# Kernel optimization log

Hardware: AMD Instinct MI355X
Metric: run time of the kernel (lower is better)

The kernel has to match this reference:

```python
import jax, jax.numpy as jnp
import numpy as np

N_NODES = 10000
N_EDGES = 640000
HIDDEN = 128
OUT = 10

def setup_inputs() -> dict:
    key = jax.random.key(0)
    k1, k2, k3, k4 = jax.random.split(key, 4)
    x = jax.random.normal(k1, (N_NODES, HIDDEN), dtype=jnp.float32)
    edge_index = jax.random.randint(k2, (2, N_EDGES), 0, N_NODES, dtype=jnp.int64)
    # ClassifierMLP2 params: Linear(2*hidden -> hidden) -> ReLU -> Linear(hidden -> out)
    W1 = jax.random.normal(k3, (2 * HIDDEN, HIDDEN), dtype=jnp.float32) / np.sqrt(2 * HIDDEN)
    b1 = jnp.zeros((HIDDEN,), dtype=jnp.float32)
    W2 = jax.random.normal(k4, (HIDDEN, OUT), dtype=jnp.float32) / np.sqrt(HIDDEN)
    b2 = jnp.zeros((OUT,), dtype=jnp.float32)
    return {"x": x, "edge_index": edge_index, "W1": W1, "b1": b1, "W2": W2, "b2": b2}

def reference(x, edge_index, W1, b1, W2, b2):
    # mix_node_features(..., node_feat_mixing='cat'): gather src/dst node
    # embeddings per edge and concatenate along feature dim -> [E, 2*H]
    src, dst = edge_index[0], edge_index[1]
    edges_x = jnp.concatenate([x[src], x[dst]], axis=-1)  # [E, 2H]
    # ClassifierMLP2 (dropout inactive at inference)
    h = jax.nn.relu(edges_x @ W1 + b1)                    # [E, H]
    return h @ W2 + b2                                    # [E, OUT]
```

## Files before the change

kernel.cpp:

```cpp
#include <hip/hip_runtime.h>


typedef _Float16 f16;
typedef _Float16 f16x8 __attribute__((ext_vector_type(8)));
typedef float    f32x4 __attribute__((ext_vector_type(4)));

#define HID  128
#define TWOH 256
#define OUTD 10

__global__ __launch_bounds__(256) void node_AB(
    const float* __restrict__ x,
    const float* __restrict__ W1,
    const float* __restrict__ b1,
    f16* __restrict__ AB,
    int n_nodes)
{
    const int t = threadIdx.x;
    const int lane = t & 63;
    const int r = lane & 15, g = lane >> 4;
    const int wv = t >> 6;
    const int n0 = blockIdx.x * 16;
    const int c0 = wv * 64;

    f16x8 w1f[4][4];
#pragma unroll
    for (int ct = 0; ct < 4; ++ct) {
        const int c = c0 + ct * 16 + r;
        const float* wp = (c < HID) ? (W1 + c) : (W1 + HID * HID + (c - HID));
#pragma unroll
        for (int st = 0; st < 4; ++st) {
            f16x8 v;
#pragma unroll
            for (int j = 0; j < 8; ++j)
                v[j] = (f16)wp[(long)(st * 32 + g * 8 + j) * HID];
            w1f[ct][st] = v;
        }
    }

    const int xrow = (n0 + r < n_nodes) ? (n0 + r) : (n_nodes - 1);
    f32x4 acc[4] = {{0,0,0,0},{0,0,0,0},{0,0,0,0},{0,0,0,0}};
#pragma unroll
    for (int st = 0; st < 4; ++st) {
        const float* xp = x + (long)xrow * HID + st * 32 + g * 8;
        const float4 x0 = *(const float4*)xp;
        const float4 x1 = *(const float4*)(xp + 4);
        f16x8 a;
        a[0] = (f16)x0.x; a[1] = (f16)x0.y; a[2] = (f16)x0.z; a[3] = (f16)x0.w;
        a[4] = (f16)x1.x; a[5] = (f16)x1.y; a[6] = (f16)x1.z; a[7] = (f16)x1.w;
#pragma unroll
        for (int ct = 0; ct < 4; ++ct)
            acc[ct] = __builtin_amdgcn_mfma_f32_16x16x32_f16(a, w1f[ct][st], acc[ct], 0, 0, 0);
    }

#pragma unroll
    for (int ct = 0; ct < 4; ++ct) {
        const int c = c0 + ct * 16 + r;
        const float bias = (c < HID) ? b1[c] : 0.f;
#pragma unroll
        for (int q = 0; q < 4; ++q) {
            const int node = n0 + g * 4 + q;
            if (node < n_nodes)
                AB[(long)node * TWOH + c] = (f16)(acc[ct][q] + bias);
        }
    }
}

__global__ __launch_bounds__(256) void edge_mlp(
    const f16* __restrict__ AB,
    const int* __restrict__ ei,
    const float* __restrict__ W2,
    const float* __restrict__ b2,
    float* __restrict__ out,
    int n_edges)
{
    const int t = threadIdx.x;
    const int lane = t & 63;
    const int r = lane & 15, g = lane >> 4;
    const int wv = t >> 6;

    const bool cok = (r < OUTD);
    const int cw = cok ? r : 0;
    f16x8 w2f[4];
#pragma unroll
    for (int st = 0; st < 4; ++st) {
        f16x8 v;
#pragma unroll
        for (int j = 0; j < 8; ++j) {
            const float w = W2[(long)(st * 32 + g * 8 + j) * OUTD + cw];
            v[j] = cok ? (f16)w : (f16)0.f;
        }
        w2f[st] = v;
    }
    const float bj = cok ? b2[r] : 0.f;

    const f16x8* __restrict__ ABv = (const f16x8*)AB;
    const long eb = (long)blockIdx.x * 256 + wv * 64;

#pragma unroll
    for (int it = 0; it < 4; ++it) {
        const long e = eb + it * 16 + r;
        const long ec = (e < n_edges) ? e : (n_edges - 1);
        const int sn = ei[ec];
        const int dn = ei[(long)n_edges + ec];

        f32x4 acc = {0, 0, 0, 0};
#pragma unroll
        for (int st = 0; st < 4; ++st) {
            const f16x8 a = ABv[(long)sn * 32 + st * 4 + g];
            const f16x8 c = ABv[(long)dn * 32 + 16 + st * 4 + g];
            f16x8 s = a + c;
            const f16x8 z = {0, 0, 0, 0, 0, 0, 0, 0};
            s = __builtin_elementwise_max(s, z);
            acc = __builtin_amdgcn_mfma_f32_16x16x32_f16(s, w2f[st], acc, 0, 0, 0);
        }

        if (cok) {
            const long er = eb + it * 16 + g * 4;
#pragma unroll
            for (int q = 0; q < 4; ++q) {
                const long ee = er + q;
                if (ee < n_edges)
                    out[ee * OUTD + r] = acc[q] + bj;
            }
        }
    }
}

extern "C" void kernel_launch(void* const* d_in, const int* in_sizes, int n_in,
                              void* d_out, int out_size, void* d_ws, size_t ws_size,
                              hipStream_t stream) {
    const float* x  = (const float*)d_in[0];
    const int*   ei = (const int*)d_in[1];
    const float* W1 = (const float*)d_in[2];
    const float* b1 = (const float*)d_in[3];
    const float* W2 = (const float*)d_in[4];
    const float* b2 = (const float*)d_in[5];
    float* out = (float*)d_out;

    const int n_nodes = in_sizes[0] / HID;
    const int n_edges = in_sizes[1] / 2;

    f16* AB = (f16*)d_ws;

    node_AB<<<(n_nodes + 15) / 16, 256, 0, stream>>>(x, W1, b1, AB, n_nodes);

    edge_mlp<<<(n_edges + 255) / 256, 256, 0, stream>>>(AB, ei, W2, b2, out, n_edges);
}
```

Before: 70.60 us.

## Prepack fp16 weight fragments and software-pipeline edge gathers

A small kernel converts W1 and W2 once per call into fp16 MFMA fragment order. The node and edge kernels then load those fragments with vector loads instead of doing strided scalar fp32 loads and converts in every block. The edge kernel now handles 8 tiles of 16 edges per wave. It preloads all indices and keeps gathers several tiles ahead of the MFMA compute, with sched_barriers to hide gather latency. This adds a third kernel launch, raises register pressure, and uses occupancy hints of 3 blocks.

Result: faster. 61.78 us (-12.5%).

```diff
diff --git a/kernel.cpp b/kernel.cpp
--- a/kernel.cpp
+++ b/kernel.cpp
@@ -9,9 +9,42 @@
 #define TWOH 256
 #define OUTD 10
 
-__global__ __launch_bounds__(256) void node_AB(
+__global__ __launch_bounds__(256) void prep_weights(
+    const float* __restrict__ W1,
+    const float* __restrict__ W2,
+    f16* __restrict__ W1P,
+    f16* __restrict__ W2P)
+{
+    const int slot = blockIdx.x * 256 + threadIdx.x;
+    if (slot < 4096) {
+        const int lane = slot & 63, i = slot >> 6;
+        const int r = lane & 15, g = lane >> 4;
+        const int wv = i >> 4, ct = (i >> 2) & 3, st = i & 3;
+        const int c = wv * 64 + ct * 16 + r;
+        f16x8 v;
+#pragma unroll
+        for (int j = 0; j < 8; ++j) {
+            const int k = st * 32 + g * 8 + j;
+            const float w = (c < HID) ? W1[k * HID + c]
+                                      : W1[(HID + k) * HID + (c - HID)];
+            v[j] = (f16)w;
+        }
+        *(f16x8*)(W1P + (long)slot * 8) = v;
+    } else if (slot < 4096 + 256) {
+        const int s2 = slot - 4096;
+        const int lane = s2 & 63, st = s2 >> 6;
+        const int r = lane & 15, g = lane >> 4;
+        f16x8 v;
+#pragma unroll
+        for (int j = 0; j < 8; ++j)
+            v[j] = (r < OUTD) ? (f16)W2[(st * 32 + g * 8 + j) * OUTD + r] : (f16)0.f;
+        *(f16x8*)(W2P + (long)s2 * 8) = v;
+    }
+}
+
+__global__ __launch_bounds__(256, 3) void node_AB(
     const float* __restrict__ x,
-    const float* __restrict__ W1,
+    const f16* __restrict__ W1P,
     const float* __restrict__ b1,
     f16* __restrict__ AB,
     int n_nodes)
@@ -21,33 +54,35 @@
     const int r = lane & 15, g = lane >> 4;
     const int wv = t >> 6;
     const int n0 = blockIdx.x * 16;
-    const int c0 = wv * 64;
-
-    f16x8 w1f[4][4];
-#pragma unroll
-    for (int ct = 0; ct < 4; ++ct) {
-        const int c = c0 + ct * 16 + r;
-        const float* wp = (c < HID) ? (W1 + c) : (W1 + HID * HID + (c - HID));
-#pragma unroll
-        for (int st = 0; st < 4; ++st) {
-            f16x8 v;
-#pragma unroll
-            for (int j = 0; j < 8; ++j)
-                v[j] = (f16)wp[(long)(st * 32 + g * 8 + j) * HID];
-            w1f[ct][st] = v;
-        }
-    }
 
     const int xrow = (n0 + r < n_nodes) ? (n0 + r) : (n_nodes - 1);
-    f32x4 acc[4] = {{0,0,0,0},{0,0,0,0},{0,0,0,0},{0,0,0,0}};
+    float4 xl[4][2];
 #pragma unroll
     for (int st = 0; st < 4; ++st) {
         const float* xp = x + (long)xrow * HID + st * 32 + g * 8;
-        const float4 x0 = *(const float4*)xp;
-        const float4 x1 = *(const float4*)(xp + 4);
+        xl[st][0] = *(const float4*)xp;
+        xl[st][1] = *(const float4*)(xp + 4);
+    }
+
+    f16x8 w1f[4][4];
+    float bias[4];
+#pragma unroll
+    for (int ct = 0; ct < 4; ++ct) {
+        const int c = wv * 64 + ct * 16 + r;
+        bias[ct] = (c < HID) ? b1[c] : 0.f;
+#pragma unroll
+        for (int st = 0; st < 4; ++st)
+            w1f[ct][st] = *(const f16x8*)(W1P + ((long)((wv * 16 + ct * 4 + st)) * 64 + lane) * 8);
+    }
+
+    f32x4 acc[4] = {{0,0,0,0},{0,0,0,0},{0,0,0,0},{0,0,0,0}};
+#pragma unroll
+    for (int st = 0; st < 4; ++st) {
         f16x8 a;
-        a[0] = (f16)x0.x; a[1] = (f16)x0.y; a[2] = (f16)x0.z; a[3] = (f16)x0.w;
-        a[4] = (f16)x1.x; a[5] = (f16)x1.y; a[6] = (f16)x1.z; a[7] = (f16)x1.w;
+        a[0] = (f16)xl[st][0].x; a[1] = (f16)xl[st][0].y;
+        a[2] = (f16)xl[st][0].z; a[3] = (f16)xl[st][0].w;
+        a[4] = (f16)xl[st][1].x; a[5] = (f16)xl[st][1].y;
+        a[6] = (f16)xl[st][1].z; a[7] = (f16)xl[st][1].w;
 #pragma unroll
         for (int ct = 0; ct < 4; ++ct)
             acc[ct] = __builtin_amdgcn_mfma_f32_16x16x32_f16(a, w1f[ct][st], acc[ct], 0, 0, 0);
@@ -55,21 +90,20 @@
 
 #pragma unroll
     for (int ct = 0; ct < 4; ++ct) {
-        const int c = c0 + ct * 16 + r;
-        const float bias = (c < HID) ? b1[c] : 0.f;
+        const int c = wv * 64 + ct * 16 + r;
 #pragma unroll
         for (int q = 0; q < 4; ++q) {
             const int node = n0 + g * 4 + q;
             if (node < n_nodes)
-                AB[(long)node * TWOH + c] = (f16)(acc[ct][q] + bias);
+                AB[(long)node * TWOH + c] = (f16)(acc[ct][q] + bias[ct]);
         }
     }
 }
 
-__global__ __launch_bounds__(256) void edge_mlp(
+__global__ __launch_bounds__(256, 3) void edge_mlp(
     const f16* __restrict__ AB,
     const int* __restrict__ ei,
-    const float* __restrict__ W2,
+    const f16* __restrict__ W2P,
     const float* __restrict__ b2,
     float* __restrict__ out,
     int n_edges)
@@ -79,52 +113,80 @@
     const int r = lane & 15, g = lane >> 4;
     const int wv = t >> 6;
 
-    const bool cok = (r < OUTD);
-    const int cw = cok ? r : 0;
     f16x8 w2f[4];
 #pragma unroll
-    for (int st = 0; st < 4; ++st) {
-        f16x8 v;
-#pragma unroll
-        for (int j = 0; j < 8; ++j) {
-            const float w = W2[(long)(st * 32 + g * 8 + j) * OUTD + cw];
-            v[j] = cok ? (f16)w : (f16)0.f;
-        }
-        w2f[st] = v;
-    }
-    const float bj = cok ? b2[r] : 0.f;
+    for (int st = 0; st < 4; ++st)
+        w2f[st] = *(const f16x8*)(W2P + ((long)st * 64 + lane) * 8);
+    const int rc = (r < OUTD) ? r : 0;
+    const float bj = b2[rc];
 
     const f16x8* __restrict__ ABv = (const f16x8*)AB;
-    const long eb = (long)blockIdx.x * 256 + wv * 64;
-
-#pragma unroll
-    for (int it = 0; it < 4; ++it) {
+    const long eb = (long)blockIdx.x * 512 + wv * 128;
+
+    int sn[8], dn[8];
+#pragma unroll
+    for (int it = 0; it < 8; ++it) {
         const long e = eb + it * 16 + r;
         const long ec = (e < n_edges) ? e : (n_edges - 1);
-        const int sn = ei[ec];
-        const int dn = ei[(long)n_edges + ec];
-
-        f32x4 acc = {0, 0, 0, 0};
-#pragma unroll
-        for (int st = 0; st < 4; ++st) {
-            const f16x8 a = ABv[(long)sn * 32 + st * 4 + g];
-            const f16x8 c = ABv[(long)dn * 32 + 16 + st * 4 + g];
-            f16x8 s = a + c;
-            const f16x8 z = {0, 0, 0, 0, 0, 0, 0, 0};
-            s = __builtin_elementwise_max(s, z);
-            acc = __builtin_amdgcn_mfma_f32_16x16x32_f16(s, w2f[st], acc, 0, 0, 0);
-        }
-
-        if (cok) {
-            const long er = eb + it * 16 + g * 4;
-#pragma unroll
-            for (int q = 0; q < 4; ++q) {
-                const long ee = er + q;
-                if (ee < n_edges)
-                    out[ee * OUTD + r] = acc[q] + bj;
-            }
-        }
-    }
+        sn[it] = ei[ec];
+        dn[it] = ei[(long)n_edges + ec];
+    }
+
+    const f16x8 zt = {0, 0, 0, 0, 0, 0, 0, 0};
+
+#define GATHER(Pa, Pc, IT)                                                  \
+    f16x8 Pa[4], Pc[4];                                                     \
+    {                                                                       \
+        const long ab_ = (long)sn[IT] * 32, bb_ = (long)dn[IT] * 32;        \
+        _Pragma("unroll")                                                   \
+        for (int st = 0; st < 4; ++st) {                                    \
+            Pa[st] = ABv[ab_ + st * 4 + g];                                 \
+            Pc[st] = ABv[bb_ + 16 + st * 4 + g];                            \
+        }                                                                   \
+    }
+
+#define COMPSTORE(Pa, Pc, IT)                                               \
+    {                                                                       \
+        f32x4 acc = {0, 0, 0, 0};                                           \
+        _Pragma("unroll")                                                   \
+        for (int st = 0; st < 4; ++st) {                                    \
+            const f16x8 s = __builtin_elementwise_max(Pa[st] + Pc[st], zt); \
+            acc = __builtin_amdgcn_mfma_f32_16x16x32_f16(s, w2f[st], acc, 0, 0, 0); \
+        }                                                                   \
+        if (r < OUTD) {                                                     \
+            _Pragma("unroll")                                               \
+            for (int q = 0; q < 4; ++q) {                                   \
+                const long ee = eb + IT * 16 + g * 4 + q;                   \
+                if (ee < n_edges) out[ee * OUTD + r] = acc[q] + bj;         \
+            }                                                               \
+        }                                                                   \
+    }
+
+    GATHER(a0, c0, 0)
+    GATHER(a1, c1, 1)
+    GATHER(a2, c2, 2)
+    __builtin_amdgcn_sched_barrier(0);
+    COMPSTORE(a0, c0, 0)
+    GATHER(a3, c3, 3)
+    __builtin_amdgcn_sched_barrier(0);
+    COMPSTORE(a1, c1, 1)
+    GATHER(a4, c4, 4)
+    __builtin_amdgcn_sched_barrier(0);
+    COMPSTORE(a2, c2, 2)
+    GATHER(a5, c5, 5)
+    __builtin_amdgcn_sched_barrier(0);
+    COMPSTORE(a3, c3, 3)
+    GATHER(a6, c6, 6)
+    __builtin_amdgcn_sched_barrier(0);
+    COMPSTORE(a4, c4, 4)
+    GATHER(a7, c7, 7)
+    __builtin_amdgcn_sched_barrier(0);
+    COMPSTORE(a5, c5, 5)
+    COMPSTORE(a6, c6, 6)
+    COMPSTORE(a7, c7, 7)
+
+#undef GATHER
+#undef COMPSTORE
 }
 
 extern "C" void kernel_launch(void* const* d_in, const int* in_sizes, int n_in,
@@ -141,9 +203,13 @@
     const int n_nodes = in_sizes[0] / HID;
     const int n_edges = in_sizes[1] / 2;
 
-    f16* AB = (f16*)d_ws;
-
-    node_AB<<<(n_nodes + 15) / 16, 256, 0, stream>>>(x, W1, b1, AB, n_nodes);
-
-    edge_mlp<<<(n_edges + 255) / 256, 256, 0, stream>>>(AB, ei, W2, b2, out, n_edges);
-}
+    f16* AB  = (f16*)d_ws;
+    f16* W1P = AB + (long)n_nodes * TWOH;
+    f16* W2P = W1P + 4096 * 8;
+
+    prep_weights<<<17, 256, 0, stream>>>(W1, W2, W1P, W2P);
+
+    node_AB<<<(n_nodes + 15) / 16, 256, 0, stream>>>(x, W1P, b1, AB, n_nodes);
+
+    edge_mlp<<<(n_edges + 511) / 512, 256, 0, stream>>>(AB, ei, W2P, b2, out, n_edges);
+}
```

## Prepack weights into fp16 MFMA fragments and shrink per-block work in both kernels

Applied to the files above, without the earlier changes.

Adds a small kernel that converts W1 and W2 once per call into fp16 fragments already laid out for MFMA, so node and edge kernels load them with one vector load per lane instead of strided scalar fp32 loads. node_AB now splits output columns across four times as many blocks, each wave computing a single 16-column tile. edge_mlp handles one 16-edge tile per wave and issues all eight gather loads up front for more memory-level parallelism, with launch bounds raised for occupancy. This costs an extra kernel launch, more blocks that each re-read x, and the weight prep on every call.

Measured after the change: 69.87 us. Within noise of the previous version (-1.0%).

```diff
diff --git a/kernel.cpp b/kernel.cpp
--- a/kernel.cpp
+++ b/kernel.cpp
@@ -9,9 +9,42 @@
 #define TWOH 256
 #define OUTD 10
 
-__global__ __launch_bounds__(256) void node_AB(
+__global__ __launch_bounds__(256) void prep_weights(
+    const float* __restrict__ W1,
+    const float* __restrict__ W2,
+    f16* __restrict__ W1P,
+    f16* __restrict__ W2P)
+{
+    const int slot = blockIdx.x * 256 + threadIdx.x;
+    if (slot < 4096) {
+        const int lane = slot & 63, i = slot >> 6;
+        const int r = lane & 15, g = lane >> 4;
+        const int T = i >> 2, st = i & 3;
+        const int c = T * 16 + r;
+        f16x8 v;
+#pragma unroll
+        for (int j = 0; j < 8; ++j) {
+            const int k = st * 32 + g * 8 + j;
+            const float w = (c < HID) ? W1[k * HID + c]
+                                      : W1[(HID + k) * HID + (c - HID)];
+            v[j] = (f16)w;
+        }
+        *(f16x8*)(W1P + (long)slot * 8) = v;
+    } else if (slot < 4096 + 256) {
+        const int s2 = slot - 4096;
+        const int lane = s2 & 63, st = s2 >> 6;
+        const int r = lane & 15, g = lane >> 4;
+        f16x8 v;
+#pragma unroll
+        for (int j = 0; j < 8; ++j)
+            v[j] = (r < OUTD) ? (f16)W2[(st * 32 + g * 8 + j) * OUTD + r] : (f16)0.f;
+        *(f16x8*)(W2P + (long)s2 * 8) = v;
+    }
+}
+
+__global__ __launch_bounds__(256, 6) void node_AB(
     const float* __restrict__ x,
-    const float* __restrict__ W1,
+    const f16* __restrict__ W1P,
     const float* __restrict__ b1,
     f16* __restrict__ AB,
     int n_nodes)
@@ -20,56 +53,48 @@
     const int lane = t & 63;
     const int r = lane & 15, g = lane >> 4;
     const int wv = t >> 6;
-    const int n0 = blockIdx.x * 16;
-    const int c0 = wv * 64;
-
-    f16x8 w1f[4][4];
-#pragma unroll
-    for (int ct = 0; ct < 4; ++ct) {
-        const int c = c0 + ct * 16 + r;
-        const float* wp = (c < HID) ? (W1 + c) : (W1 + HID * HID + (c - HID));
-#pragma unroll
-        for (int st = 0; st < 4; ++st) {
-            f16x8 v;
-#pragma unroll
-            for (int j = 0; j < 8; ++j)
-                v[j] = (f16)wp[(long)(st * 32 + g * 8 + j) * HID];
-            w1f[ct][st] = v;
-        }
-    }
+    const int n0 = (blockIdx.x >> 2) * 16;
+    const int T = (blockIdx.x & 3) * 4 + wv;
+    const int c = T * 16 + r;
 
     const int xrow = (n0 + r < n_nodes) ? (n0 + r) : (n_nodes - 1);
-    f32x4 acc[4] = {{0,0,0,0},{0,0,0,0},{0,0,0,0},{0,0,0,0}};
+    float4 xl[4][2];
 #pragma unroll
     for (int st = 0; st < 4; ++st) {
         const float* xp = x + (long)xrow * HID + st * 32 + g * 8;
-        const float4 x0 = *(const float4*)xp;
-        const float4 x1 = *(const float4*)(xp + 4);
+        xl[st][0] = *(const float4*)xp;
+        xl[st][1] = *(const float4*)(xp + 4);
+    }
+
+    f16x8 w1f[4];
+#pragma unroll
+    for (int st = 0; st < 4; ++st)
+        w1f[st] = *(const f16x8*)(W1P + ((long)(T * 4 + st) * 64 + lane) * 8);
+    const float bias = (c < HID) ? b1[c] : 0.f;
+
+    f32x4 acc = {0, 0, 0, 0};
+#pragma unroll
+    for (int st = 0; st < 4; ++st) {
         f16x8 a;
-        a[0] = (f16)x0.x; a[1] = (f16)x0.y; a[2] = (f16)x0.z; a[3] = (f16)x0.w;
-        a[4] = (f16)x1.x; a[5] = (f16)x1.y; a[6] = (f16)x1.z; a[7] = (f16)x1.w;
-#pragma unroll
-        for (int ct = 0; ct < 4; ++ct)
-            acc[ct] = __builtin_amdgcn_mfma_f32_16x16x32_f16(a, w1f[ct][st], acc[ct], 0, 0, 0);
+        a[0] = (f16)xl[st][0].x; a[1] = (f16)xl[st][0].y;
+        a[2] = (f16)xl[st][0].z; a[3] = (f16)xl[st][0].w;
+        a[4] = (f16)xl[st][1].x; a[5] = (f16)xl[st][1].y;
+        a[6] = (f16)xl[st][1].z; a[7] = (f16)xl[st][1].w;
+        acc = __builtin_amdgcn_mfma_f32_16x16x32_f16(a, w1f[st], acc, 0, 0, 0);
     }
 
 #pragma unroll
-    for (int ct = 0; ct < 4; ++ct) {
-        const int c = c0 + ct * 16 + r;
-        const float bias = (c < HID) ? b1[c] : 0.f;
-#pragma unroll
-        for (int q = 0; q < 4; ++q) {
-            const int node = n0 + g * 4 + q;
-            if (node < n_nodes)
-                AB[(long)node * TWOH + c] = (f16)(acc[ct][q] + bias);
-        }
+    for (int q = 0; q < 4; ++q) {
+        const int node = n0 + g * 4 + q;
+        if (node < n_nodes)
+            AB[(long)node * TWOH + c] = (f16)(acc[q] + bias);
     }
 }
 
-__global__ __launch_bounds__(256) void edge_mlp(
+__global__ __launch_bounds__(256, 6) void edge_mlp(
     const f16* __restrict__ AB,
     const int* __restrict__ ei,
-    const float* __restrict__ W2,
+    const f16* __restrict__ W2P,
     const float* __restrict__ b2,
     float* __restrict__ out,
     int n_edges)
@@ -79,50 +104,47 @@
     const int r = lane & 15, g = lane >> 4;
     const int wv = t >> 6;
 
-    const bool cok = (r < OUTD);
-    const int cw = cok ? r : 0;
+    const long eb = (long)blockIdx.x * 64 + wv * 16;
+    const long e = eb + r;
+    const long ec = (e < n_edges) ? e : (n_edges - 1);
+    const int sn = ei[ec];
+    const int dn = ei[(long)n_edges + ec];
+
+    const f16* pa = AB + ((long)sn * TWOH + g * 8);
+    const f16* pb = AB + ((long)dn * TWOH + HID + g * 8);
+    f16x8 a0 = *(const f16x8*)pa;
+    f16x8 a1 = *(const f16x8*)(pa + 32);
+    f16x8 a2 = *(const f16x8*)(pa + 64);
+    f16x8 a3 = *(const f16x8*)(pa + 96);
+    f16x8 c0 = *(const f16x8*)pb;
+    f16x8 c1 = *(const f16x8*)(pb + 32);
+    f16x8 c2 = *(const f16x8*)(pb + 64);
+    f16x8 c3 = *(const f16x8*)(pb + 96);
+
     f16x8 w2f[4];
 #pragma unroll
-    for (int st = 0; st < 4; ++st) {
-        f16x8 v;
+    for (int st = 0; st < 4; ++st)
+        w2f[st] = *(const f16x8*)(W2P + ((long)st * 64 + lane) * 8);
+    const float bj = b2[(r < OUTD) ? r : 0];
+
+    const f16x8 zt = {0, 0, 0, 0, 0, 0, 0, 0};
+    f32x4 acc = {0, 0, 0, 0};
+    f16x8 s;
+    s = __builtin_elementwise_max(a0 + c0, zt);
+    acc = __builtin_amdgcn_mfma_f32_16x16x32_f16(s, w2f[0], acc, 0, 0, 0);
+    s = __builtin_elementwise_max(a1 + c1, zt);
+    acc = __builtin_amdgcn_mfma_f32_16x16x32_f16(s, w2f[1], acc, 0, 0, 0);
+    s = __builtin_elementwise_max(a2 + c2, zt);
+    acc = __builtin_amdgcn_mfma_f32_16x16x32_f16(s, w2f[2], acc, 0, 0, 0);
+    s = __builtin_elementwise_max(a3 + c3, zt);
+    acc = __builtin_amdgcn_mfma_f32_16x16x32_f16(s, w2f[3], acc, 0, 0, 0);
+
+    if (r < OUTD) {
 #pragma unroll
-        for (int j = 0; j < 8; ++j) {
-            const float w = W2[(long)(st * 32 + g * 8 + j) * OUTD + cw];
-            v[j] = cok ? (f16)w : (f16)0.f;
-        }
-        w2f[st] = v;
-    }
-    const float bj = cok ? b2[r] : 0.f;
-
-    const f16x8* __restrict__ ABv = (const f16x8*)AB;
-    const long eb = (long)blockIdx.x * 256 + wv * 64;
-
-#pragma unroll
-    for (int it = 0; it < 4; ++it) {
-        const long e = eb + it * 16 + r;
-        const long ec = (e < n_edges) ? e : (n_edges - 1);
-        const int sn = ei[ec];
-        const int dn = ei[(long)n_edges + ec];
-
-        f32x4 acc = {0, 0, 0, 0};
-#pragma unroll
-        for (int st = 0; st < 4; ++st) {
-            const f16x8 a = ABv[(long)sn * 32 + st * 4 + g];
-            const f16x8 c = ABv[(long)dn * 32 + 16 + st * 4 + g];
-            f16x8 s = a + c;
-            const f16x8 z = {0, 0, 0, 0, 0, 0, 0, 0};
-            s = __builtin_elementwise_max(s, z);
-            acc = __builtin_amdgcn_mfma_f32_16x16x32_f16(s, w2f[st], acc, 0, 0, 0);
-        }
-
-        if (cok) {
-            const long er = eb + it * 16 + g * 4;
-#pragma unroll
-            for (int q = 0; q < 4; ++q) {
-                const long ee = er + q;
-                if (ee < n_edges)
-                    out[ee * OUTD + r] = acc[q] + bj;
-            }
+        for (int q = 0; q < 4; ++q) {
+            const long ee = eb + g * 4 + q;
+            if (ee < n_edges)
+                out[ee * OUTD + r] = acc[q] + bj;
         }
     }
 }
@@ -141,9 +163,13 @@
     const int n_nodes = in_sizes[0] / HID;
     const int n_edges = in_sizes[1] / 2;
 
-    f16* AB = (f16*)d_ws;
+    f16* AB  = (f16*)d_ws;
+    f16* W1P = AB + (long)n_nodes * TWOH;
+    f16* W2P = W1P + 4096 * 8;
 
-    node_AB<<<(n_nodes + 15) / 16, 256, 0, stream>>>(x, W1, b1, AB, n_nodes);
+    prep_weights<<<17, 256, 0, stream>>>(W1, W2, W1P, W2P);
 
-    edge_mlp<<<(n_edges + 255) / 256, 256, 0, stream>>>(AB, ei, W2, b2, out, n_edges);
+    node_AB<<<((n_nodes + 15) / 16) * 4, 256, 0, stream>>>(x, W1P, b1, AB, n_nodes);
+
+    edge_mlp<<<(n_edges + 63) / 64, 256, 0, stream>>>(AB, ei, W2P, b2, out, n_edges);
 }
```
